# Optimization experiments

Measured on AMD Instinct MI355X. Metric: run time of the kernel, lower is better.

Reference implementation:

```python
import jax, jax.numpy as jnp
import numpy as np

E, D_MODEL, D_HIDDEN, TOK_PER_EXP = 64, 1024, 4096, 128


def setup_inputs() -> dict:
    key = jax.random.key(0)
    k1, k2, k3 = jax.random.split(key, 3)
    n_tokens = E * TOK_PER_EXP  # 8192
    inputs = jax.random.normal(k1, (n_tokens, D_MODEL), dtype=jnp.float32)
    # torch nn.Linear weights are [out_features, in_features]
    w1 = jax.random.normal(k2, (E, D_HIDDEN, D_MODEL), dtype=jnp.float32) * (1.0 / np.sqrt(D_MODEL))
    w2 = jax.random.normal(k3, (E, D_MODEL, D_HIDDEN), dtype=jnp.float32) * (1.0 / np.sqrt(D_HIDDEN))
    splits = np.full((E,), TOK_PER_EXP, dtype=np.int64)  # concrete host-side sizes, as in torch .tolist()
    return {"inputs": inputs, "w1": w1, "w2": w2, "splits": splits}


def reference(inputs, w1, w2, splits):
    # splits is a concrete (host) int array: chunk sizes along token dim, expert i uses splits[i % E].
    sizes = [int(s) for s in np.asarray(splits)]
    offsets = np.concatenate([[0], np.cumsum(sizes)])
    n_exp = w1.shape[0]
    outs = []
    for i, m in enumerate(sizes):  # loop over fixed expert list (structurally distinct weights)
        e = i % n_exp
        x = jax.lax.dynamic_slice_in_dim(inputs, int(offsets[i]), m, axis=0)  # [m, d_model]
        h = jax.nn.relu(x @ w1[e].T)          # [m, d_hidden]
        outs.append(h @ w2[e].T)              # [m, d_model]
    return jnp.concatenate(outs, axis=0)       # [N, d_model]
```

## Files before the change

### kernel.cpp

```cpp
#include <hip/hip_runtime.h>
#include <hip/hip_bf16.h>


typedef __attribute__((ext_vector_type(8))) short bf16x8;
typedef __attribute__((ext_vector_type(4))) float f32x4;
typedef __attribute__((ext_vector_type(4))) unsigned int u32x4;

#define N_EXPERTS 64
#define DM 1024
#define DH 4096
#define TOKS 128

__device__ __forceinline__ unsigned f2u(float f) {
    union { float f; unsigned u; } v; v.f = f; return v.u;
}
__device__ __forceinline__ unsigned short f2bf(float f) {
    return (unsigned short)((f2u(f) + 0x8000u) >> 16);
}
__device__ __forceinline__ unsigned pack2(float lo, float hi) {
    return ((f2u(lo) + 0x8000u) >> 16) | ((f2u(hi) + 0x8000u) & 0xFFFF0000u);
}

__global__ __launch_bounds__(256)
void cvt_bf16(const float* __restrict__ in, unsigned* __restrict__ outp, int n8) {
    int i = blockIdx.x * blockDim.x + threadIdx.x;
    if (i >= n8) return;
    const f32x4* p = (const f32x4*)in + (size_t)i * 2;
    f32x4 a = p[0], b = p[1];
    u32x4 o = { pack2(a[0], a[1]), pack2(a[2], a[3]),
                pack2(b[0], b[1]), pack2(b[2], b[3]) };
    *((u32x4*)outp + i) = o;
}

template<int N, int K, bool RELU_OUT_BF16>
__global__ __launch_bounds__(256, 2)
void moe_gemm(const unsigned short* __restrict__ Ab, const float* __restrict__ Bp,
              void* __restrict__ Cp, int nwg_per_xcd)
{
    constexpr int BK = 32;
    constexpr int NT = K / BK;
    constexpr int NTILES = N / 128;

    __shared__ unsigned short sA[2][128][BK];
    __shared__ unsigned short sB[2][128][BK];

    const int tid = threadIdx.x;
    const int bid = (blockIdx.x & 7) * nwg_per_xcd + (blockIdx.x >> 3);
    const int e   = bid / NTILES;
    const int nt  = bid % NTILES;

    const int lane = tid & 63;
    const int w    = tid >> 6;
    const int wr   = w >> 1;
    const int wc   = w & 1;
    const int lrow = lane & 15;
    const int kq   = lane >> 4;

    const int arow = tid >> 2;
    const int ac   = tid & 3;
    const int aswz = (arow >> 1) & 3;

    const unsigned short* aBase = Ab + (size_t)(e * TOKS + arow) * K + ac * 8;
    const float*          bBase = Bp + ((size_t)e * N + (size_t)nt * 128 + arow) * K + ac * 8;

    const int offk = ((kq ^ ((lrow >> 1) & 3))) * 8;

    f32x4 acc[4][4];
    #pragma unroll
    for (int i = 0; i < 4; ++i)
        #pragma unroll
        for (int n = 0; n < 4; ++n)
            #pragma unroll
            for (int q = 0; q < 4; ++q) acc[i][n][q] = 0.f;

    struct SetA { u32x4 a[2]; };
    struct SetB { f32x4 b[4]; };
    SetA sa0, sa1, sa2, sa3;
    SetB sb0, sb1, sb2, sb3;

    auto LOAD = [&](int t, SetA& A, SetB& B) {
        #pragma unroll
        for (int j = 0; j < 2; ++j)
            A.a[j] = *(const u32x4*)(aBase + (size_t)j * 64 * K + t * BK);
        #pragma unroll
        for (int j = 0; j < 2; ++j) {
            const f32x4* p = (const f32x4*)(bBase + (size_t)j * 64 * K + t * BK);
            B.b[2 * j]     = __builtin_nontemporal_load(p);
            B.b[2 * j + 1] = __builtin_nontemporal_load(p + 1);
        }
    };

    auto WRITE = [&](int buf, SetA& A, SetB& B) {
        const int c8 = (ac ^ aswz) * 8;
        #pragma unroll
        for (int j = 0; j < 2; ++j)
            *(u32x4*)&sA[buf][arow + j * 64][c8] = A.a[j];
        #pragma unroll
        for (int j = 0; j < 2; ++j) {
            f32x4 lo = B.b[2 * j], hi = B.b[2 * j + 1];
            u32x4 u = { pack2(lo[0], lo[1]), pack2(lo[2], lo[3]),
                        pack2(hi[0], hi[1]), pack2(hi[2], hi[3]) };
            *(u32x4*)&sB[buf][arow + j * 64][c8] = u;
        }
    };

    auto COMPUTE = [&](int buf) {
        bf16x8 af[4], bfr[4];
        #pragma unroll
        for (int i = 0; i < 4; ++i)
            af[i] = *(const bf16x8*)&sA[buf][wr * 64 + i * 16 + lrow][offk];
        #pragma unroll
        for (int n = 0; n < 4; ++n)
            bfr[n] = *(const bf16x8*)&sB[buf][wc * 64 + n * 16 + lrow][offk];
        #pragma unroll
        for (int i = 0; i < 4; ++i)
            #pragma unroll
            for (int n = 0; n < 4; ++n)
                acc[i][n] = __builtin_amdgcn_mfma_f32_16x16x32_bf16(af[i], bfr[n], acc[i][n], 0, 0, 0);
    };

    LOAD(0, sa0, sb0);
    LOAD(1, sa1, sb1);
    LOAD(2, sa2, sb2);
    WRITE(0, sa0, sb0);
    asm volatile("s_waitcnt lgkmcnt(0)" ::: "memory");
    __builtin_amdgcn_s_barrier();

    for (int t = 0; t < NT; t += 4) {
        if (t + 3 < NT) LOAD(t + 3, sa3, sb3);
        COMPUTE(0);
        WRITE(1, sa1, sb1);
        asm volatile("s_waitcnt lgkmcnt(0)" ::: "memory");
        __builtin_amdgcn_s_barrier();

        if (t + 4 < NT) LOAD(t + 4, sa0, sb0);
        COMPUTE(1);
        if (t + 2 < NT) WRITE(0, sa2, sb2);
        asm volatile("s_waitcnt lgkmcnt(0)" ::: "memory");
        __builtin_amdgcn_s_barrier();

        if (t + 5 < NT) LOAD(t + 5, sa1, sb1);
        COMPUTE(0);
        if (t + 3 < NT) WRITE(1, sa3, sb3);
        asm volatile("s_waitcnt lgkmcnt(0)" ::: "memory");
        __builtin_amdgcn_s_barrier();

        if (t + 6 < NT) LOAD(t + 6, sa2, sb2);
        COMPUTE(1);
        if (t + 4 < NT) WRITE(0, sa0, sb0);
        asm volatile("s_waitcnt lgkmcnt(0)" ::: "memory");
        __builtin_amdgcn_s_barrier();
    }

    const size_t crow0 = (size_t)e * TOKS;
    if constexpr (RELU_OUT_BF16) {
        unsigned short* C = (unsigned short*)Cp;
        #pragma unroll
        for (int i = 0; i < 4; ++i)
            #pragma unroll
            for (int n = 0; n < 4; ++n)
                #pragma unroll
                for (int q = 0; q < 4; ++q) {
                    const int row = wr * 64 + i * 16 + kq * 4 + q;
                    const int col = nt * 128 + wc * 64 + n * 16 + lrow;
                    C[(crow0 + row) * N + col] = f2bf(fmaxf(acc[i][n][q], 0.f));
                }
    } else {
        float* C = (float*)Cp;
        #pragma unroll
        for (int i = 0; i < 4; ++i)
            #pragma unroll
            for (int n = 0; n < 4; ++n)
                #pragma unroll
                for (int q = 0; q < 4; ++q) {
                    const int row = wr * 64 + i * 16 + kq * 4 + q;
                    const int col = nt * 128 + wc * 64 + n * 16 + lrow;
                    C[(crow0 + row) * N + col] = acc[i][n][q];
                }
    }
}

extern "C" void kernel_launch(void* const* d_in, const int* in_sizes, int n_in,
                              void* d_out, int out_size, void* d_ws, size_t ws_size,
                              hipStream_t stream) {
    const float* inputs = (const float*)d_in[0];
    const float* w1     = (const float*)d_in[1];
    const float* w2     = (const float*)d_in[2];

    unsigned short* h  = (unsigned short*)d_ws;
    unsigned short* xb = (unsigned short*)((char*)d_ws + (size_t)64 * 1024 * 1024);
    float* out = (float*)d_out;

    const int n8 = (TOKS * N_EXPERTS) * DM / 8;
    cvt_bf16<<<dim3(n8 / 256), dim3(256), 0, stream>>>(inputs, (unsigned*)xb, n8);

    moe_gemm<DH, DM, true><<<dim3(N_EXPERTS * (DH / 128)), dim3(256), 0, stream>>>(
        xb, w1, h, N_EXPERTS * (DH / 128) / 8);
    moe_gemm<DM, DH, false><<<dim3(N_EXPERTS * (DM / 128)), dim3(256), 0, stream>>>(
        h, w2, out, N_EXPERTS * (DM / 128) / 8);
}
```

Baseline: 529.1 us.

## Halve GEMM N-tile to 64 and raise occupancy with shallower prefetch

Shrinks the per-workgroup output tile from 128x128 to 128x64, halving B staging and accumulators, and doubles the launched workgroups. The register prefetch pipeline is reduced from three tiles ahead to one, and launch bounds request four workgroups per CU. The aim is more concurrent waves and better CU fill for the weight-streaming, bandwidth-bound GEMMs. The trade-off is that the bf16 activation tile is read twice as often and there is less latency hiding per wave.

```diff
diff --git a/kernel.cpp b/kernel.cpp
--- a/kernel.cpp
+++ b/kernel.cpp
@@ -33,16 +33,16 @@
 }
 
 template<int N, int K, bool RELU_OUT_BF16>
-__global__ __launch_bounds__(256, 2)
+__global__ __launch_bounds__(256, 4)
 void moe_gemm(const unsigned short* __restrict__ Ab, const float* __restrict__ Bp,
               void* __restrict__ Cp, int nwg_per_xcd)
 {
     constexpr int BK = 32;
     constexpr int NT = K / BK;
-    constexpr int NTILES = N / 128;
+    constexpr int NTILES = N / 64;
 
     __shared__ unsigned short sA[2][128][BK];
-    __shared__ unsigned short sB[2][128][BK];
+    __shared__ unsigned short sB[2][64][BK];
 
     const int tid = threadIdx.x;
     const int bid = (blockIdx.x & 7) * nwg_per_xcd + (blockIdx.x >> 3);
@@ -61,33 +61,34 @@
     const int aswz = (arow >> 1) & 3;
 
     const unsigned short* aBase = Ab + (size_t)(e * TOKS + arow) * K + ac * 8;
-    const float*          bBase = Bp + ((size_t)e * N + (size_t)nt * 128 + arow) * K + ac * 8;
 
-    const int offk = ((kq ^ ((lrow >> 1) & 3))) * 8;
+    const int brow = tid >> 2;
+    const int bc   = tid & 3;
+    const int bswz = (brow >> 1) & 3;
+    const float* bBase = Bp + ((size_t)e * N + (size_t)nt * 64 + brow) * K + bc * 8;
 
-    f32x4 acc[4][4];
+    const int offk = (kq ^ ((lrow >> 1) & 3)) * 8;
+
+    f32x4 acc[4][2];
     #pragma unroll
     for (int i = 0; i < 4; ++i)
         #pragma unroll
-        for (int n = 0; n < 4; ++n)
+        for (int n = 0; n < 2; ++n)
             #pragma unroll
             for (int q = 0; q < 4; ++q) acc[i][n][q] = 0.f;
 
     struct SetA { u32x4 a[2]; };
-    struct SetB { f32x4 b[4]; };
-    SetA sa0, sa1, sa2, sa3;
-    SetB sb0, sb1, sb2, sb3;
+    struct SetB { f32x4 b[2]; };
+    SetA sa0, sa1;
+    SetB sb0, sb1;
 
     auto LOAD = [&](int t, SetA& A, SetB& B) {
         #pragma unroll
         for (int j = 0; j < 2; ++j)
             A.a[j] = *(const u32x4*)(aBase + (size_t)j * 64 * K + t * BK);
-        #pragma unroll
-        for (int j = 0; j < 2; ++j) {
-            const f32x4* p = (const f32x4*)(bBase + (size_t)j * 64 * K + t * BK);
-            B.b[2 * j]     = __builtin_nontemporal_load(p);
-            B.b[2 * j + 1] = __builtin_nontemporal_load(p + 1);
-        }
+        const f32x4* p = (const f32x4*)(bBase + t * BK);
+        B.b[0] = __builtin_nontemporal_load(p);
+        B.b[1] = __builtin_nontemporal_load(p + 1);
     };
 
     auto WRITE = [&](int buf, SetA& A, SetB& B) {
@@ -95,59 +96,42 @@
         #pragma unroll
         for (int j = 0; j < 2; ++j)
             *(u32x4*)&sA[buf][arow + j * 64][c8] = A.a[j];
-        #pragma unroll
-        for (int j = 0; j < 2; ++j) {
-            f32x4 lo = B.b[2 * j], hi = B.b[2 * j + 1];
-            u32x4 u = { pack2(lo[0], lo[1]), pack2(lo[2], lo[3]),
-                        pack2(hi[0], hi[1]), pack2(hi[2], hi[3]) };
-            *(u32x4*)&sB[buf][arow + j * 64][c8] = u;
-        }
+        u32x4 u = { pack2(B.b[0][0], B.b[0][1]), pack2(B.b[0][2], B.b[0][3]),
+                    pack2(B.b[1][0], B.b[1][1]), pack2(B.b[1][2], B.b[1][3]) };
+        *(u32x4*)&sB[buf][brow][(bc ^ bswz) * 8] = u;
     };
 
     auto COMPUTE = [&](int buf) {
-        bf16x8 af[4], bfr[4];
+        bf16x8 af[4], bfr[2];
         #pragma unroll
         for (int i = 0; i < 4; ++i)
             af[i] = *(const bf16x8*)&sA[buf][wr * 64 + i * 16 + lrow][offk];
         #pragma unroll
-        for (int n = 0; n < 4; ++n)
-            bfr[n] = *(const bf16x8*)&sB[buf][wc * 64 + n * 16 + lrow][offk];
+        for (int n = 0; n < 2; ++n)
+            bfr[n] = *(const bf16x8*)&sB[buf][wc * 32 + n * 16 + lrow][offk];
         #pragma unroll
         for (int i = 0; i < 4; ++i)
             #pragma unroll
-            for (int n = 0; n < 4; ++n)
+            for (int n = 0; n < 2; ++n)
                 acc[i][n] = __builtin_amdgcn_mfma_f32_16x16x32_bf16(af[i], bfr[n], acc[i][n], 0, 0, 0);
     };
 
     LOAD(0, sa0, sb0);
     LOAD(1, sa1, sb1);
-    LOAD(2, sa2, sb2);
     WRITE(0, sa0, sb0);
     asm volatile("s_waitcnt lgkmcnt(0)" ::: "memory");
     __builtin_amdgcn_s_barrier();
 
-    for (int t = 0; t < NT; t += 4) {
-        if (t + 3 < NT) LOAD(t + 3, sa3, sb3);
+    for (int t = 0; t < NT; t += 2) {
+        if (t + 2 < NT) LOAD(t + 2, sa0, sb0);
         COMPUTE(0);
-        WRITE(1, sa1, sb1);
+        if (t + 1 < NT) WRITE(1, sa1, sb1);
         asm volatile("s_waitcnt lgkmcnt(0)" ::: "memory");
         __builtin_amdgcn_s_barrier();
 
-        if (t + 4 < NT) LOAD(t + 4, sa0, sb0);
+        if (t + 3 < NT) LOAD(t + 3, sa1, sb1);
         COMPUTE(1);
-        if (t + 2 < NT) WRITE(0, sa2, sb2);
-        asm volatile("s_waitcnt lgkmcnt(0)" ::: "memory");
-        __builtin_amdgcn_s_barrier();
-
-        if (t + 5 < NT) LOAD(t + 5, sa1, sb1);
-        COMPUTE(0);
-        if (t + 3 < NT) WRITE(1, sa3, sb3);
-        asm volatile("s_waitcnt lgkmcnt(0)" ::: "memory");
-        __builtin_amdgcn_s_barrier();
-
-        if (t + 6 < NT) LOAD(t + 6, sa2, sb2);
-        COMPUTE(1);
-        if (t + 4 < NT) WRITE(0, sa0, sb0);
+        if (t + 2 < NT) WRITE(0, sa0, sb0);
         asm volatile("s_waitcnt lgkmcnt(0)" ::: "memory");
         __builtin_amdgcn_s_barrier();
     }
@@ -158,11 +142,11 @@
         #pragma unroll
         for (int i = 0; i < 4; ++i)
             #pragma unroll
-            for (int n = 0; n < 4; ++n)
+            for (int n = 0; n < 2; ++n)
                 #pragma unroll
                 for (int q = 0; q < 4; ++q) {
                     const int row = wr * 64 + i * 16 + kq * 4 + q;
-                    const int col = nt * 128 + wc * 64 + n * 16 + lrow;
+                    const int col = nt * 64 + wc * 32 + n * 16 + lrow;
                     C[(crow0 + row) * N + col] = f2bf(fmaxf(acc[i][n][q], 0.f));
                 }
     } else {
@@ -170,11 +154,11 @@
         #pragma unroll
         for (int i = 0; i < 4; ++i)
             #pragma unroll
-            for (int n = 0; n < 4; ++n)
+            for (int n = 0; n < 2; ++n)
                 #pragma unroll
                 for (int q = 0; q < 4; ++q) {
                     const int row = wr * 64 + i * 16 + kq * 4 + q;
-                    const int col = nt * 128 + wc * 64 + n * 16 + lrow;
+                    const int col = nt * 64 + wc * 32 + n * 16 + lrow;
                     C[(crow0 + row) * N + col] = acc[i][n][q];
                 }
     }
@@ -194,8 +178,8 @@
     const int n8 = (TOKS * N_EXPERTS) * DM / 8;
     cvt_bf16<<<dim3(n8 / 256), dim3(256), 0, stream>>>(inputs, (unsigned*)xb, n8);
 
-    moe_gemm<DH, DM, true><<<dim3(N_EXPERTS * (DH / 128)), dim3(256), 0, stream>>>(
-        xb, w1, h, N_EXPERTS * (DH / 128) / 8);
-    moe_gemm<DM, DH, false><<<dim3(N_EXPERTS * (DM / 128)), dim3(256), 0, stream>>>(
-        h, w2, out, N_EXPERTS * (DM / 128) / 8);
+    moe_gemm<DH, DM, true><<<dim3(N_EXPERTS * (DH / 64)), dim3(256), 0, stream>>>(
+        xb, w1, h, N_EXPERTS * (DH / 64) / 8);
+    moe_gemm<DM, DH, false><<<dim3(N_EXPERTS * (DM / 64)), dim3(256), 0, stream>>>(
+        h, w2, out, N_EXPERTS * (DM / 64) / 8);
 }
```

After: 622.1 us. +17.6%, slower.
